# Kernel optimization log

Hardware: AMD Instinct MI355X
Metric: run time of the kernel (lower is better)

The kernel has to match this reference:

```python
import jax, jax.numpy as jnp
from jax import lax
import numpy as np

IN, H, OUT = 14, 28, 2
B, T = 4096, 512


def setup_inputs() -> dict:
    key = jax.random.key(0)
    ks = jax.random.split(key, 7)
    s_ih = 1.0 / np.sqrt(H)
    return {
        "x": jax.random.normal(ks[0], (B, T, IN), dtype=jnp.float32),
        "W_ih": jax.random.uniform(ks[1], (4 * H, IN), jnp.float32, -s_ih, s_ih),
        "W_hh": jax.random.uniform(ks[2], (4 * H, H), jnp.float32, -s_ih, s_ih),
        "b_ih": jax.random.uniform(ks[3], (4 * H,), jnp.float32, -s_ih, s_ih),
        "b_hh": jax.random.uniform(ks[4], (4 * H,), jnp.float32, -s_ih, s_ih),
        "W_out": jax.random.uniform(ks[5], (OUT, H), jnp.float32, -s_ih, s_ih),
        "b_out": jax.random.uniform(ks[6], (OUT,), jnp.float32, -s_ih, s_ih),
    }


def reference(x, W_ih, W_hh, b_ih, b_hh, W_out, b_out):
    # x: [B, T, IN]; PyTorch LSTM gate order: i, f, g, o
    b, h = x.shape[0], W_hh.shape[1]
    h0 = jnp.zeros((b, h), x.dtype)
    c0 = jnp.zeros((b, h), x.dtype)
    # precompute input projection for all timesteps: [T, B, 4H]
    xg = jnp.einsum('bti,gi->tbg', x, W_ih) + b_ih + b_hh

    def step(carry, xt):
        hp, cp = carry
        gates = xt + hp @ W_hh.T            # [B, 4H]
        i, f, g, o = jnp.split(gates, 4, axis=-1)
        c = jax.nn.sigmoid(f) * cp + jax.nn.sigmoid(i) * jnp.tanh(g)
        hn = jax.nn.sigmoid(o) * jnp.tanh(c)
        return (hn, c), None

    (hT, _), _ = lax.scan(step, (h0, c0), xg)
    # out = Linear(r_out[:, -1, :]) == Linear(h_T)
    return hT @ W_out.T + b_out
```

## Files before the change

kernel.cpp:

```cpp
#include <hip/hip_runtime.h>


#define T_STEPS 512
#define BATCH   4096
#define IN_F    14
#define HID     28
#define OUT_N   2
#define MB      16
#define TC      16
#define NCHUNK  (T_STEPS / TC)
#define HPITCH  40
#define NTHR    512
#define XREGS   ((MB * TC * IN_F) / NTHR)

typedef __attribute__((ext_vector_type(8))) short  short8;
typedef __attribute__((ext_vector_type(4))) float  float4v;

#define L1 1.4426950408889634f
#define L2 2.8853900817779268f

__device__ __forceinline__ unsigned short f2bf(float f) {
    union { float f; unsigned int u; } v; v.f = f;
    unsigned int r = (v.u + 0x7FFFu + ((v.u >> 16) & 1u)) >> 16;
    return (unsigned short)r;
}

__device__ __forceinline__ void gate4(const float4v pr, float& c, float& hf) {
    float ei = __builtin_amdgcn_exp2f(pr[0] * (-L1));
    float ef = __builtin_amdgcn_exp2f(pr[1] * (-L1));
    float eg = __builtin_amdgcn_exp2f(pr[2] * (-L2));
    float eo = __builtin_amdgcn_exp2f(pr[3] * (-L1));
    float av = 1.0f + ei, bv = 1.0f + ef, dv = 1.0f + eg, vv = 1.0f + eo;
    float pd  = av * dv;
    float pqv = pd * bv;
    float rv  = __builtin_amdgcn_rcpf(pqv);
    float sfv = pd * rv;
    float igv = (1.0f - eg) * bv * rv;
    c = fmaf(sfv, c, igv);
    float ec = __builtin_amdgcn_exp2f(c * (-L2));
    float wv = 1.0f + ec;
    float r2 = __builtin_amdgcn_rcpf(vv * wv);
    hf = (1.0f - ec) * r2;
}

__global__ __launch_bounds__(512, 1)
void lstm_f8(const float* __restrict__ x,
             const float* __restrict__ W_ih,
             const float* __restrict__ W_hh,
             const float* __restrict__ b_ih,
             const float* __restrict__ b_hh,
             const float* __restrict__ W_out,
             const float* __restrict__ b_out,
             float* __restrict__ out) {
    __shared__ __align__(16) short h_a[2][MB][HPITCH];
    __shared__ __align__(16) short x_a[2][TC][MB][HPITCH];
    __shared__ float hfin[MB][HID];

    const int tid = threadIdx.x;
    const int w   = tid >> 6;
    const int l   = tid & 63;
    const int q   = l >> 4;
    const int m   = l & 15;
    const int b0  = blockIdx.x * MB;
    const bool act = (w < 7);
    const int u   = 4 * w + q;

    short8  Ah = {0,0,0,0,0,0,0,0}, Ax = {0,0,0,0,0,0,0,0};
    float4v bias = {0.0f, 0.0f, 0.0f, 0.0f};
    if (act) {
        const int unit = 4 * w + (m >> 2);
        const int wrow = (m & 3) * HID + unit;
        #pragma unroll
        for (int j = 0; j < 8; ++j) {
            const int k = 8 * q + j;
            float wh = (k < HID)  ? W_hh[wrow * HID + k]  : 0.0f;
            float wx = (k < IN_F) ? W_ih[wrow * IN_F + k] : 0.0f;
            Ah[j] = (short)f2bf(wh);
            Ax[j] = (short)f2bf(wx);
        }
        #pragma unroll
        for (int j = 0; j < 4; ++j)
            bias[j] = b_ih[j * HID + u] + b_hh[j * HID + u];
    }

    for (int k = tid; k < 2 * MB * HPITCH; k += NTHR) ((short*)h_a)[k] = 0;
    for (int k = tid; k < 2 * TC * MB * HPITCH; k += NTHR) ((short*)x_a)[k] = 0;

    const float* xbase = x + (long)b0 * T_STEPS * IN_F;
    float xr[XREGS];
    #pragma unroll
    for (int k = 0; k < XREGS; ++k) {
        const int u2 = tid + NTHR * k;
        const int bb = u2 / (TC * IN_F);
        const int r  = u2 - bb * (TC * IN_F);
        xr[k] = xbase[(long)bb * T_STEPS * IN_F + r];
    }
    __syncthreads();

    float c = 0.0f, hf = 0.0f;
    int rb = 0;
    float4v accx = bias;

    for (int ch = 0; ch < NCHUNK; ++ch) {
        const int buf = ch & 1;
        #pragma unroll
        for (int k = 0; k < XREGS; ++k) {
            const int u2 = tid + NTHR * k;
            const int bb = u2 / (TC * IN_F);
            const int r  = u2 - bb * (TC * IN_F);
            const int t  = r / IN_F;
            const int f  = r - t * IN_F;
            x_a[buf][t][bb][f] = (short)f2bf(xr[k]);
        }
        if (ch + 1 < NCHUNK) {
            #pragma unroll
            for (int k = 0; k < XREGS; ++k) {
                const int u2 = tid + NTHR * k;
                const int bb = u2 / (TC * IN_F);
                const int r  = u2 - bb * (TC * IN_F);
                xr[k] = xbase[(long)bb * T_STEPS * IN_F + (ch + 1) * TC * IN_F + r];
            }
        }
        __syncthreads();

        if (act) {
            short8 bx0 = *(const short8*)&x_a[buf][0][m][8 * q];
            accx = __builtin_amdgcn_mfma_f32_16x16x32_bf16(Ax, bx0, bias, 0, 0, 0);
        }

        for (int tt = 0; tt < TC; ++tt) {
            if (act) {
                short8 bh = *(const short8*)&h_a[rb][m][8 * q];
                float4v acc = __builtin_amdgcn_mfma_f32_16x16x32_bf16(Ah, bh, accx, 0, 0, 0);
                if (tt + 1 < TC) {
                    short8 bxn = *(const short8*)&x_a[buf][tt + 1][m][8 * q];
                    accx = __builtin_amdgcn_mfma_f32_16x16x32_bf16(Ax, bxn, bias, 0, 0, 0);
                }
                gate4(acc, c, hf);
                ((short*)&h_a[rb ^ 1][m][0])[u] = (short)f2bf(hf);
            }
            rb ^= 1;
            __syncthreads();
        }
    }

    if (act) hfin[m][u] = hf;
    __syncthreads();
    if (tid < MB * OUT_N) {
        const int o  = tid & 1;
        const int bb = tid >> 1;
        float s = b_out[o];
        #pragma unroll
        for (int k = 0; k < HID; ++k)
            s = fmaf(hfin[bb][k], W_out[o * HID + k], s);
        out[(b0 + bb) * OUT_N + o] = s;
    }
}

extern "C" void kernel_launch(void* const* d_in, const int* in_sizes, int n_in,
                              void* d_out, int out_size, void* d_ws, size_t ws_size,
                              hipStream_t stream) {
    const float* x     = (const float*)d_in[0];
    const float* W_ih  = (const float*)d_in[1];
    const float* W_hh  = (const float*)d_in[2];
    const float* b_ih  = (const float*)d_in[3];
    const float* b_hh  = (const float*)d_in[4];
    const float* W_out = (const float*)d_in[5];
    const float* b_out = (const float*)d_in[6];
    float* out = (float*)d_out;

    lstm_f8<<<BATCH / MB, NTHR, 0, stream>>>(
        x, W_ih, W_hh, b_ih, b_hh, W_out, b_out, out);
}
```

Before: 273.9 us.

## Halve batch per block, pack two hidden units per wave with dual MFMAs

```diff
diff --git a/kernel.cpp b/kernel.cpp
--- a/kernel.cpp
+++ b/kernel.cpp
@@ -6,11 +6,11 @@
 #define IN_F    14
 #define HID     28
 #define OUT_N   2
-#define MB      16
+#define MB      8
 #define TC      16
 #define NCHUNK  (T_STEPS / TC)
 #define HPITCH  40
-#define NTHR    512
+#define NTHR    256
 #define XREGS   ((MB * TC * IN_F) / NTHR)
 
 typedef __attribute__((ext_vector_type(8))) short  short8;
@@ -23,6 +23,12 @@
     union { float f; unsigned int u; } v; v.f = f;
     unsigned int r = (v.u + 0x7FFFu + ((v.u >> 16) & 1u)) >> 16;
     return (unsigned short)r;
+}
+
+__device__ __forceinline__ int cvtpk_bf16(float lo, float hi) {
+    int r;
+    asm("v_cvt_pk_bf16_f32 %0, %1, %2" : "=v"(r) : "v"(lo), "v"(hi));
+    return r;
 }
 
 __device__ __forceinline__ void gate4(const float4v pr, float& c, float& hf) {
@@ -43,8 +49,8 @@
     hf = (1.0f - ec) * r2;
 }
 
-__global__ __launch_bounds__(512, 1)
-void lstm_f8(const float* __restrict__ x,
+__global__ __launch_bounds__(256, 2)
+void lstm_d2(const float* __restrict__ x,
              const float* __restrict__ W_ih,
              const float* __restrict__ W_hh,
              const float* __restrict__ b_ih,
@@ -61,26 +67,36 @@
     const int l   = tid & 63;
     const int q   = l >> 4;
     const int m   = l & 15;
+    const int bb8 = m & 7;
+    const int sel = m >> 3;
+    const int u0  = 8 * w + 2 * q;
+    const int u   = u0 + sel;
     const int b0  = blockIdx.x * MB;
-    const bool act = (w < 7);
-    const int u   = 4 * w + q;
 
-    short8  Ah = {0,0,0,0,0,0,0,0}, Ax = {0,0,0,0,0,0,0,0};
-    float4v bias = {0.0f, 0.0f, 0.0f, 0.0f};
-    if (act) {
-        const int unit = 4 * w + (m >> 2);
-        const int wrow = (m & 3) * HID + unit;
+    short8  Ah[2], Ax[2];
+    float4v bias[2];
+    #pragma unroll
+    for (int s = 0; s < 2; ++s) {
+        const int ua = 8 * w + 2 * (m >> 2) + s;
+        const bool vr = (ua < HID);
+        const int wrow = (m & 3) * HID + (vr ? ua : 0);
+        short8 vh = {0,0,0,0,0,0,0,0}, vx = {0,0,0,0,0,0,0,0};
         #pragma unroll
         for (int j = 0; j < 8; ++j) {
             const int k = 8 * q + j;
-            float wh = (k < HID)  ? W_hh[wrow * HID + k]  : 0.0f;
-            float wx = (k < IN_F) ? W_ih[wrow * IN_F + k] : 0.0f;
-            Ah[j] = (short)f2bf(wh);
-            Ax[j] = (short)f2bf(wx);
+            float wh = (vr && k < HID)  ? W_hh[wrow * HID + k]  : 0.0f;
+            float wx = (vr && k < IN_F) ? W_ih[wrow * IN_F + k] : 0.0f;
+            vh[j] = (short)f2bf(wh);
+            vx[j] = (short)f2bf(wx);
         }
+        Ah[s] = vh;
+        Ax[s] = vx;
+        const int us = u0 + s;
+        float4v bv;
         #pragma unroll
         for (int j = 0; j < 4; ++j)
-            bias[j] = b_ih[j * HID + u] + b_hh[j * HID + u];
+            bv[j] = (us < HID) ? (b_ih[j * HID + us] + b_hh[j * HID + us]) : 0.0f;
+        bias[s] = bv;
     }
 
     for (int k = tid; k < 2 * MB * HPITCH; k += NTHR) ((short*)h_a)[k] = 0;
@@ -97,9 +113,9 @@
     }
     __syncthreads();
 
+    const bool wact = (m < 8) && (u0 + 1 < HID);
     float c = 0.0f, hf = 0.0f;
-    int rb = 0;
-    float4v accx = bias;
+    float4v accx0, accx1;
 
     for (int ch = 0; ch < NCHUNK; ++ch) {
         const int buf = ch & 1;
@@ -123,28 +139,36 @@
         }
         __syncthreads();
 
-        if (act) {
-            short8 bx0 = *(const short8*)&x_a[buf][0][m][8 * q];
-            accx = __builtin_amdgcn_mfma_f32_16x16x32_bf16(Ax, bx0, bias, 0, 0, 0);
+        {
+            short8 bx0 = *(const short8*)&x_a[buf][0][bb8][8 * q];
+            accx0 = __builtin_amdgcn_mfma_f32_16x16x32_bf16(Ax[0], bx0, bias[0], 0, 0, 0);
+            accx1 = __builtin_amdgcn_mfma_f32_16x16x32_bf16(Ax[1], bx0, bias[1], 0, 0, 0);
         }
 
+        #pragma unroll
         for (int tt = 0; tt < TC; ++tt) {
-            if (act) {
-                short8 bh = *(const short8*)&h_a[rb][m][8 * q];
-                float4v acc = __builtin_amdgcn_mfma_f32_16x16x32_bf16(Ah, bh, accx, 0, 0, 0);
-                if (tt + 1 < TC) {
-                    short8 bxn = *(const short8*)&x_a[buf][tt + 1][m][8 * q];
-                    accx = __builtin_amdgcn_mfma_f32_16x16x32_bf16(Ax, bxn, bias, 0, 0, 0);
-                }
-                gate4(acc, c, hf);
-                ((short*)&h_a[rb ^ 1][m][0])[u] = (short)f2bf(hf);
+            const int rd = tt & 1;
+            const int wr = rd ^ 1;
+            short8 bh = *(const short8*)&h_a[rd][bb8][8 * q];
+            float4v a0 = __builtin_amdgcn_mfma_f32_16x16x32_bf16(Ah[0], bh, accx0, 0, 0, 0);
+            float4v a1 = __builtin_amdgcn_mfma_f32_16x16x32_bf16(Ah[1], bh, accx1, 0, 0, 0);
+            if (tt + 1 < TC) {
+                short8 bxn = *(const short8*)&x_a[buf][tt + 1][bb8][8 * q];
+                accx0 = __builtin_amdgcn_mfma_f32_16x16x32_bf16(Ax[0], bxn, bias[0], 0, 0, 0);
+                accx1 = __builtin_amdgcn_mfma_f32_16x16x32_bf16(Ax[1], bxn, bias[1], 0, 0, 0);
             }
-            rb ^= 1;
+            float4v acc;
+            #pragma unroll
+            for (int j = 0; j < 4; ++j) acc[j] = sel ? a1[j] : a0[j];
+            gate4(acc, c, hf);
+            int hpart = __builtin_amdgcn_ds_swizzle(__builtin_bit_cast(int, hf), 0x201F);
+            if (wact)
+                *(int*)&h_a[wr][m][u0] = cvtpk_bf16(hf, __builtin_bit_cast(float, hpart));
             __syncthreads();
         }
     }
 
-    if (act) hfin[m][u] = hf;
+    if (u < HID) hfin[bb8][u] = hf;
     __syncthreads();
     if (tid < MB * OUT_N) {
         const int o  = tid & 1;
@@ -169,6 +193,6 @@
     const float* b_out = (const float*)d_in[6];
     float* out = (float*)d_out;
 
-    lstm_f8<<<BATCH / MB, NTHR, 0, stream>>>(
+    lstm_d2<<<BATCH / MB, NTHR, 0, stream>>>(
         x, W_ih, W_hh, b_ih, b_hh, W_out, b_out, out);
 }
```

Measured after the change: 282.1 us. 1.03x slower.

## Restructure LSTM into single-wave blocks to eliminate per-step barriers

Applied to the files above, without the earlier changes.

```diff
diff --git a/kernel.cpp b/kernel.cpp
--- a/kernel.cpp
+++ b/kernel.cpp
@@ -6,12 +6,13 @@
 #define IN_F    14
 #define HID     28
 #define OUT_N   2
-#define MB      16
-#define TC      16
+#define MB      4
+#define TC      8
 #define NCHUNK  (T_STEPS / TC)
 #define HPITCH  40
-#define NTHR    512
+#define NTHR    64
 #define XREGS   ((MB * TC * IN_F) / NTHR)
+#define NT      7
 
 typedef __attribute__((ext_vector_type(8))) short  short8;
 typedef __attribute__((ext_vector_type(4))) float  float4v;
@@ -43,8 +44,8 @@
     hf = (1.0f - ec) * r2;
 }
 
-__global__ __launch_bounds__(512, 1)
-void lstm_f8(const float* __restrict__ x,
+__global__ __launch_bounds__(64, 1)
+void lstm_w1(const float* __restrict__ x,
              const float* __restrict__ W_ih,
              const float* __restrict__ W_hh,
              const float* __restrict__ b_ih,
@@ -52,103 +53,124 @@
              const float* __restrict__ W_out,
              const float* __restrict__ b_out,
              float* __restrict__ out) {
-    __shared__ __align__(16) short h_a[2][MB][HPITCH];
-    __shared__ __align__(16) short x_a[2][TC][MB][HPITCH];
+    __shared__ __align__(16) short h_a[MB][HPITCH];
+    __shared__ __align__(16) short x_a[TC][MB][HPITCH];
     __shared__ float hfin[MB][HID];
 
-    const int tid = threadIdx.x;
-    const int w   = tid >> 6;
-    const int l   = tid & 63;
-    const int q   = l >> 4;
-    const int m   = l & 15;
-    const int b0  = blockIdx.x * MB;
-    const bool act = (w < 7);
-    const int u   = 4 * w + q;
+    const int l  = threadIdx.x;
+    const int q  = l >> 4;
+    const int m  = l & 15;
+    const int b3 = m & 3;
+    const int cp = m >> 2;
+    const int b0 = blockIdx.x * MB;
 
-    short8  Ah = {0,0,0,0,0,0,0,0}, Ax = {0,0,0,0,0,0,0,0};
-    float4v bias = {0.0f, 0.0f, 0.0f, 0.0f};
-    if (act) {
-        const int unit = 4 * w + (m >> 2);
-        const int wrow = (m & 3) * HID + unit;
+    const bool cb0 = (cp & 1) != 0;
+    const bool cb1 = (cp & 2) != 0;
+    const int  u1  = 4 * cp + q;
+    const int  u2  = 16 + 4 * cp + q;
+    const bool v2  = (cp < 3);
+
+    short8  Ah[NT], Ax[NT];
+    float4v bias[NT];
+    #pragma unroll
+    for (int ts = 0; ts < NT; ++ts) {
+        const int uA   = 4 * ts + cp;
+        const int wrow = (m & 3) * HID + uA;
+        short8 vh, vx;
         #pragma unroll
         for (int j = 0; j < 8; ++j) {
             const int k = 8 * q + j;
             float wh = (k < HID)  ? W_hh[wrow * HID + k]  : 0.0f;
             float wx = (k < IN_F) ? W_ih[wrow * IN_F + k] : 0.0f;
-            Ah[j] = (short)f2bf(wh);
-            Ax[j] = (short)f2bf(wx);
+            vh[j] = (short)f2bf(wh);
+            vx[j] = (short)f2bf(wx);
         }
+        Ah[ts] = vh;
+        Ax[ts] = vx;
+        const int uC = 4 * ts + q;
+        float4v bv;
         #pragma unroll
         for (int j = 0; j < 4; ++j)
-            bias[j] = b_ih[j * HID + u] + b_hh[j * HID + u];
+            bv[j] = b_ih[j * HID + uC] + b_hh[j * HID + uC];
+        bias[ts] = bv;
     }
 
-    for (int k = tid; k < 2 * MB * HPITCH; k += NTHR) ((short*)h_a)[k] = 0;
-    for (int k = tid; k < 2 * TC * MB * HPITCH; k += NTHR) ((short*)x_a)[k] = 0;
+    for (int k = l; k < MB * HPITCH; k += NTHR) ((short*)h_a)[k] = 0;
+    for (int k = l; k < TC * MB * HPITCH; k += NTHR) ((short*)x_a)[k] = 0;
 
     const float* xbase = x + (long)b0 * T_STEPS * IN_F;
     float xr[XREGS];
     #pragma unroll
     for (int k = 0; k < XREGS; ++k) {
-        const int u2 = tid + NTHR * k;
-        const int bb = u2 / (TC * IN_F);
-        const int r  = u2 - bb * (TC * IN_F);
+        const int u  = l + NTHR * k;
+        const int bb = u / (TC * IN_F);
+        const int r  = u - bb * (TC * IN_F);
         xr[k] = xbase[(long)bb * T_STEPS * IN_F + r];
     }
-    __syncthreads();
 
-    float c = 0.0f, hf = 0.0f;
-    int rb = 0;
-    float4v accx = bias;
+    float c1 = 0.0f, c2 = 0.0f, h1 = 0.0f, h2 = 0.0f;
+    float4v accx[NT];
 
     for (int ch = 0; ch < NCHUNK; ++ch) {
-        const int buf = ch & 1;
         #pragma unroll
         for (int k = 0; k < XREGS; ++k) {
-            const int u2 = tid + NTHR * k;
-            const int bb = u2 / (TC * IN_F);
-            const int r  = u2 - bb * (TC * IN_F);
+            const int u  = l + NTHR * k;
+            const int bb = u / (TC * IN_F);
+            const int r  = u - bb * (TC * IN_F);
             const int t  = r / IN_F;
             const int f  = r - t * IN_F;
-            x_a[buf][t][bb][f] = (short)f2bf(xr[k]);
+            x_a[t][bb][f] = (short)f2bf(xr[k]);
         }
         if (ch + 1 < NCHUNK) {
             #pragma unroll
             for (int k = 0; k < XREGS; ++k) {
-                const int u2 = tid + NTHR * k;
-                const int bb = u2 / (TC * IN_F);
-                const int r  = u2 - bb * (TC * IN_F);
+                const int u  = l + NTHR * k;
+                const int bb = u / (TC * IN_F);
+                const int r  = u - bb * (TC * IN_F);
                 xr[k] = xbase[(long)bb * T_STEPS * IN_F + (ch + 1) * TC * IN_F + r];
             }
         }
-        __syncthreads();
-
-        if (act) {
-            short8 bx0 = *(const short8*)&x_a[buf][0][m][8 * q];
-            accx = __builtin_amdgcn_mfma_f32_16x16x32_bf16(Ax, bx0, bias, 0, 0, 0);
+        {
+            short8 bx0 = *(const short8*)&x_a[0][b3][8 * q];
+            #pragma unroll
+            for (int ts = 0; ts < NT; ++ts)
+                accx[ts] = __builtin_amdgcn_mfma_f32_16x16x32_bf16(Ax[ts], bx0, bias[ts], 0, 0, 0);
         }
 
+        #pragma unroll
         for (int tt = 0; tt < TC; ++tt) {
-            if (act) {
-                short8 bh = *(const short8*)&h_a[rb][m][8 * q];
-                float4v acc = __builtin_amdgcn_mfma_f32_16x16x32_bf16(Ah, bh, accx, 0, 0, 0);
-                if (tt + 1 < TC) {
-                    short8 bxn = *(const short8*)&x_a[buf][tt + 1][m][8 * q];
-                    accx = __builtin_amdgcn_mfma_f32_16x16x32_bf16(Ax, bxn, bias, 0, 0, 0);
-                }
-                gate4(acc, c, hf);
-                ((short*)&h_a[rb ^ 1][m][0])[u] = (short)f2bf(hf);
+            short8 bh = *(const short8*)&h_a[b3][8 * q];
+            float4v acc[NT];
+            #pragma unroll
+            for (int ts = 0; ts < NT; ++ts)
+                acc[ts] = __builtin_amdgcn_mfma_f32_16x16x32_bf16(Ah[ts], bh, accx[ts], 0, 0, 0);
+            if (tt + 1 < TC) {
+                short8 bxn = *(const short8*)&x_a[tt + 1][b3][8 * q];
+                #pragma unroll
+                for (int ts = 0; ts < NT; ++ts)
+                    accx[ts] = __builtin_amdgcn_mfma_f32_16x16x32_bf16(Ax[ts], bxn, bias[ts], 0, 0, 0);
             }
-            rb ^= 1;
-            __syncthreads();
+            float4v a1, a2;
+            #pragma unroll
+            for (int j = 0; j < 4; ++j) {
+                float s01 = cb0 ? acc[1][j] : acc[0][j];
+                float s23 = cb0 ? acc[3][j] : acc[2][j];
+                a1[j] = cb1 ? s23 : s01;
+                float s45 = cb0 ? acc[5][j] : acc[4][j];
+                a2[j] = cb1 ? acc[6][j] : s45;
+            }
+            gate4(a1, c1, h1);
+            gate4(a2, c2, h2);
+            ((short*)&h_a[b3][0])[u1] = (short)f2bf(h1);
+            if (v2) ((short*)&h_a[b3][0])[u2] = (short)f2bf(h2);
         }
     }
 
-    if (act) hfin[m][u] = hf;
-    __syncthreads();
-    if (tid < MB * OUT_N) {
-        const int o  = tid & 1;
-        const int bb = tid >> 1;
+    hfin[b3][u1] = h1;
+    if (v2) hfin[b3][u2] = h2;
+    if (l < MB * OUT_N) {
+        const int o  = l & 1;
+        const int bb = l >> 1;
         float s = b_out[o];
         #pragma unroll
         for (int k = 0; k < HID; ++k)
@@ -169,6 +191,6 @@
     const float* b_out = (const float*)d_in[6];
     float* out = (float*)d_out;
 
-    lstm_f8<<<BATCH / MB, NTHR, 0, stream>>>(
+    lstm_w1<<<BATCH / MB, NTHR, 0, stream>>>(
         x, W_ih, W_hh, b_ih, b_hh, W_out, b_out, out);
 }
```

Result: slower. 336.9 us (+23.0%).
